# Kernel optimization log

Measured on AMD Instinct MI355X. Metric: run time of the kernel, lower is better.

Reference implementation:

```python
import jax, jax.numpy as jnp
import numpy as np
from jax import lax

PATCH_SIZE = 7


def _census_weight(patch_size, dtype=jnp.float32):
    oc = patch_size * patch_size
    w = np.eye(oc).reshape((patch_size, patch_size, 1, oc))
    w = np.transpose(w, (3, 2, 0, 1))  # [oc, 1, p, p] (OIHW)
    return jnp.asarray(w, dtype=dtype)


def _transform(t, w, patch_size):
    # t: [B, C, H, W] -> grayscale [B, 1, H, W]
    g = t.mean(axis=1, keepdims=True)
    pad = patch_size // 2
    # identity conv gathers the p*p neighborhood into channels: [B, p*p, H, W]
    patches = lax.conv_general_dilated(
        g, w.astype(g.dtype), window_strides=(1, 1),
        padding=[(pad, pad), (pad, pad)],
        dimension_numbers=('NCHW', 'OIHW', 'NCHW'))
    loc_diff = patches - g
    return loc_diff / jnp.sqrt(0.81 + loc_diff ** 2)


def _valid_mask(x, patch_size):
    pad = patch_size // 2
    b, _, h, w = x.shape
    inner = jnp.ones((b, 1, h - 2 * pad, w - 2 * pad), dtype=x.dtype)
    return jnp.pad(inner, ((0, 0), (0, 0), (pad, pad), (pad, pad)))


def setup_inputs() -> dict:
    key = jax.random.key(0)
    k1, k2 = jax.random.split(key)
    x = jax.random.uniform(k1, (8, 3, 256, 256), dtype=jnp.float32)
    y = jax.random.uniform(k2, (8, 3, 256, 256), dtype=jnp.float32)
    return {"x": x, "y": y}


def reference(x, y):
    w = _census_weight(PATCH_SIZE, x.dtype)
    ld_x = _transform(x, w, PATCH_SIZE)
    ld_y = _transform(y, w, PATCH_SIZE)
    diff = ld_x - lax.stop_gradient(ld_y)  # matches .detach()
    dist = (diff ** 2 / (0.1 + diff ** 2)).mean(axis=1, keepdims=True)
    mask = _valid_mask(x, PATCH_SIZE)
    return (dist * mask).mean()
```

## Files before the change

### kernel.cpp

```cpp
#include <hip/hip_runtime.h>

#define HW    256
#define TILE  32
#define HALO  3
#define PSIDE (TILE + 2*HALO)
#define LST   40

__global__ __launch_bounds__(256, 2) void census_loss_kernel(
    const float* __restrict__ x, const float* __restrict__ y,
    float* __restrict__ out)
{
    __shared__ __attribute__((aligned(16))) float sgx[PSIDE][LST];
    __shared__ __attribute__((aligned(16))) float sgy[PSIDE][LST];

    const int b   = blockIdx.z;
    const int ti0 = blockIdx.y * TILE;
    const int tj0 = blockIdx.x * TILE;

    const float* xb = x + (size_t)b * 3 * HW * HW;
    const float* yb = y + (size_t)b * 3 * HW * HW;

    const int tid = threadIdx.x;
    const float third = 1.0f / 3.0f;

    for (int li = tid; li < PSIDE * PSIDE; li += 256) {
        int r = li / PSIDE;
        int c = li - r * PSIDE;
        int gi = ti0 + r - HALO;
        int gj = tj0 + c - HALO;
        float gx = 0.0f, gy = 0.0f;
        if ((unsigned)gi < HW && (unsigned)gj < HW) {
            int o = gi * HW + gj;
            gx = (xb[o] + xb[o + HW*HW] + xb[o + 2*HW*HW]) * third;
            gy = (yb[o] + yb[o + HW*HW] + yb[o + 2*HW*HW]) * third;
        }
        sgx[r][c] = gx;
        sgy[r][c] = gy;
    }
    __syncthreads();

    const int cq = tid & 7;
    const int R  = tid >> 3;
    const int C0 = cq * 4;

    float acc[4] = {0.0f, 0.0f, 0.0f, 0.0f};
    float cxv[4], cyv[4];

    #define ROW_BODY(AR, GETC)                                                 \
    {                                                                          \
        const float4 a0 = *(const float4*)&sgx[(AR)][C0];                      \
        const float4 a1 = *(const float4*)&sgx[(AR)][C0 + 4];                  \
        const float4 a2 = *(const float4*)&sgx[(AR)][C0 + 8];                  \
        const float4 b0 = *(const float4*)&sgy[(AR)][C0];                      \
        const float4 b1 = *(const float4*)&sgy[(AR)][C0 + 4];                  \
        const float4 b2 = *(const float4*)&sgy[(AR)][C0 + 8];                  \
        const float wx[12] = {a0.x,a0.y,a0.z,a0.w, a1.x,a1.y,a1.z,a1.w,        \
                              a2.x,a2.y,a2.z,a2.w};                            \
        const float wy[12] = {b0.x,b0.y,b0.z,b0.w, b1.x,b1.y,b1.z,b1.w,        \
                              b2.x,b2.y,b2.z,b2.w};                            \
        if (GETC) {                                                            \
            _Pragma("unroll")                                                  \
            for (int p = 0; p < 4; ++p) { cxv[p] = wx[p+3]; cyv[p] = wy[p+3]; }\
        }                                                                      \
        _Pragma("unroll")                                                      \
        for (int p = 0; p < 4; ++p) {                                          \
            _Pragma("unroll")                                                  \
            for (int dx = 0; dx < 7; ++dx) {                                   \
                float ux = wx[p + dx] - cxv[p];                                \
                float uy = wy[p + dx] - cyv[p];                                \
                float fx = ux * __builtin_amdgcn_rsqf(__builtin_fmaf(ux, ux, 0.81f)); \
                float fy = uy * __builtin_amdgcn_rsqf(__builtin_fmaf(uy, uy, 0.81f)); \
                float d  = fx - fy;                                            \
                acc[p] += __builtin_amdgcn_rcpf(__builtin_fmaf(d, d, 0.1f));   \
            }                                                                  \
        }                                                                      \
    }

    ROW_BODY(R + 3, true)
    #pragma unroll
    for (int t = 0; t < 6; ++t) {
        const int dy = (t < 3) ? t : t + 1;
        ROW_BODY(R + dy, false)
    }
    #undef ROW_BODY

    const int gi = ti0 + R;
    const bool rowok = (gi >= HALO) & (gi < HW - HALO);
    float a = 0.0f;
    #pragma unroll
    for (int p = 0; p < 4; ++p) {
        const int gj = tj0 + C0 + p;
        a += (rowok & (gj >= HALO) & (gj < HW - HALO)) ? acc[p] : 0.0f;
    }

    #pragma unroll
    for (int off = 32; off > 0; off >>= 1)
        a += __shfl_down(a, off, 64);

    __shared__ float wsum[4];
    const int lane = tid & 63;
    const int wid  = tid >> 6;
    if (lane == 0) wsum[wid] = a;
    __syncthreads();
    if (tid == 0) {
        float s = wsum[0] + wsum[1] + wsum[2] + wsum[3];
        const float scale = 1.0f / (49.0f * 8.0f * 256.0f * 256.0f);
        float contrib = -0.1f * scale * s;
        if (blockIdx.x == 0 && blockIdx.y == 0 && blockIdx.z == 0) {
            contrib += 62500.0f / 65536.0f;
        }
        atomicAdd(out, contrib);
    }
}

extern "C" void kernel_launch(void* const* d_in, const int* in_sizes, int n_in,
                              void* d_out, int out_size, void* d_ws, size_t ws_size,
                              hipStream_t stream) {
    const float* x = (const float*)d_in[0];
    const float* y = (const float*)d_in[1];
    float* out = (float*)d_out;

    hipMemsetAsync(out, 0, sizeof(float) * out_size, stream);

    dim3 grid(HW / TILE, HW / TILE, 8);
    dim3 block(256);
    census_loss_kernel<<<grid, block, 0, stream>>>(x, y, out);
}
```

Measured before the change: 78.50 us.

## Exploit pairwise symmetry of census distance to halve neighbor evaluations

The per-pair term for pixel p and offset d equals the term for pixel p+d and offset -d, so each unordered pair is computed once. The result is credited to both pixels through separate accumulators, masked by per-column and per-row validity. Only the forward half-window (3 offsets in the centre row, 3 full rows below) is evaluated, and the centre self-pair is dropped and folded into the constant term. This roughly halves the rsq/rcp transcendental work in exchange for extra accumulators, mask FMAs and register pressure.

```diff
diff --git a/kernel.cpp b/kernel.cpp
--- a/kernel.cpp
+++ b/kernel.cpp
@@ -26,11 +26,11 @@
     for (int li = tid; li < PSIDE * PSIDE; li += 256) {
         int r = li / PSIDE;
         int c = li - r * PSIDE;
-        int gi = ti0 + r - HALO;
-        int gj = tj0 + c - HALO;
+        int gi_ = ti0 + r - HALO;
+        int gj_ = tj0 + c - HALO;
         float gx = 0.0f, gy = 0.0f;
-        if ((unsigned)gi < HW && (unsigned)gj < HW) {
-            int o = gi * HW + gj;
+        if ((unsigned)gi_ < HW && (unsigned)gj_ < HW) {
+            int o = gi_ * HW + gj_;
             gx = (xb[o] + xb[o + HW*HW] + xb[o + 2*HW*HW]) * third;
             gy = (yb[o] + yb[o + HW*HW] + yb[o + 2*HW*HW]) * third;
         }
@@ -43,55 +43,91 @@
     const int R  = tid >> 3;
     const int C0 = cq * 4;
 
-    float acc[4] = {0.0f, 0.0f, 0.0f, 0.0f};
-    float cxv[4], cyv[4];
+    const int gi = ti0 + R;
 
-    #define ROW_BODY(AR, GETC)                                                 \
-    {                                                                          \
-        const float4 a0 = *(const float4*)&sgx[(AR)][C0];                      \
-        const float4 a1 = *(const float4*)&sgx[(AR)][C0 + 4];                  \
-        const float4 a2 = *(const float4*)&sgx[(AR)][C0 + 8];                  \
-        const float4 b0 = *(const float4*)&sgy[(AR)][C0];                      \
-        const float4 b1 = *(const float4*)&sgy[(AR)][C0 + 4];                  \
-        const float4 b2 = *(const float4*)&sgy[(AR)][C0 + 8];                  \
-        const float wx[12] = {a0.x,a0.y,a0.z,a0.w, a1.x,a1.y,a1.z,a1.w,        \
-                              a2.x,a2.y,a2.z,a2.w};                            \
-        const float wy[12] = {b0.x,b0.y,b0.z,b0.w, b1.x,b1.y,b1.z,b1.w,        \
-                              b2.x,b2.y,b2.z,b2.w};                            \
-        if (GETC) {                                                            \
-            _Pragma("unroll")                                                  \
-            for (int p = 0; p < 4; ++p) { cxv[p] = wx[p+3]; cyv[p] = wy[p+3]; }\
-        }                                                                      \
-        _Pragma("unroll")                                                      \
-        for (int p = 0; p < 4; ++p) {                                          \
-            _Pragma("unroll")                                                  \
-            for (int dx = 0; dx < 7; ++dx) {                                   \
-                float ux = wx[p + dx] - cxv[p];                                \
-                float uy = wy[p + dx] - cyv[p];                                \
-                float fx = ux * __builtin_amdgcn_rsqf(__builtin_fmaf(ux, ux, 0.81f)); \
-                float fy = uy * __builtin_amdgcn_rsqf(__builtin_fmaf(uy, uy, 0.81f)); \
-                float d  = fx - fy;                                            \
-                acc[p] += __builtin_amdgcn_rcpf(__builtin_fmaf(d, d, 0.1f));   \
-            }                                                                  \
-        }                                                                      \
+    float colTf[12];
+    #pragma unroll
+    for (int q = 0; q < 12; ++q) {
+        int jq = tj0 + C0 + q - 3;
+        colTf[q] = (jq >= HALO && jq < HW - HALO) ? 1.0f : 0.0f;
+    }
+    const float rowCf = (gi >= HALO && gi < HW - HALO) ? 1.0f : 0.0f;
+
+    float accC[4] = {0.f, 0.f, 0.f, 0.f};
+    float accT = 0.0f;
+    float cx[4], cy[4];
+
+    #define LOADW(AR)                                                   \
+        { const float4 a0 = *(const float4*)&sgx[(AR)][C0];             \
+          const float4 a1 = *(const float4*)&sgx[(AR)][C0 + 4];         \
+          const float4 a2 = *(const float4*)&sgx[(AR)][C0 + 8];         \
+          const float4 b0 = *(const float4*)&sgy[(AR)][C0];             \
+          const float4 b1 = *(const float4*)&sgy[(AR)][C0 + 4];         \
+          const float4 b2 = *(const float4*)&sgy[(AR)][C0 + 8];         \
+          wx[0]=a0.x; wx[1]=a0.y; wx[2]=a0.z;  wx[3]=a0.w;              \
+          wx[4]=a1.x; wx[5]=a1.y; wx[6]=a1.z;  wx[7]=a1.w;              \
+          wx[8]=a2.x; wx[9]=a2.y; wx[10]=a2.z; wx[11]=a2.w;             \
+          wy[0]=b0.x; wy[1]=b0.y; wy[2]=b0.z;  wy[3]=b0.w;              \
+          wy[4]=b1.x; wy[5]=b1.y; wy[6]=b1.z;  wy[7]=b1.w;              \
+          wy[8]=b2.x; wy[9]=b2.y; wy[10]=b2.z; wy[11]=b2.w; }
+
+    #define BODY(Q, P)                                                    \
+        { float ux = wx[Q] - cx[P];                                       \
+          float uy = wy[Q] - cy[P];                                       \
+          float fx = ux * __builtin_amdgcn_rsqf(__builtin_fmaf(ux,ux,0.81f)); \
+          float fy = uy * __builtin_amdgcn_rsqf(__builtin_fmaf(uy,uy,0.81f)); \
+          float d  = fx - fy;                                             \
+          float G  = __builtin_amdgcn_rcpf(__builtin_fmaf(d,d,0.1f));     \
+          accC[P] += G;                                                   \
+          aq[Q]   += G; }
+
+    {
+        float wx[12], wy[12];
+        LOADW(R + 3)
+        #pragma unroll
+        for (int p = 0; p < 4; ++p) { cx[p] = wx[p + 3]; cy[p] = wy[p + 3]; }
+        float aq[12];
+        #pragma unroll
+        for (int q = 0; q < 12; ++q) aq[q] = 0.0f;
+        #pragma unroll
+        for (int p = 0; p < 4; ++p) {
+            #pragma unroll
+            for (int dx = 1; dx <= 3; ++dx)
+                BODY(p + 3 + dx, p)
+        }
+        float t = 0.0f;
+        #pragma unroll
+        for (int q = 4; q <= 9; ++q) t = __builtin_fmaf(aq[q], colTf[q], t);
+        accT = __builtin_fmaf(rowCf, t, accT);
     }
 
-    ROW_BODY(R + 3, true)
     #pragma unroll
-    for (int t = 0; t < 6; ++t) {
-        const int dy = (t < 3) ? t : t + 1;
-        ROW_BODY(R + dy, false)
+    for (int ddy = 1; ddy <= 3; ++ddy) {
+        float wx[12], wy[12];
+        LOADW(R + 3 + ddy)
+        float aq[12];
+        #pragma unroll
+        for (int q = 0; q < 12; ++q) aq[q] = 0.0f;
+        #pragma unroll
+        for (int p = 0; p < 4; ++p) {
+            #pragma unroll
+            for (int dx = 0; dx <= 6; ++dx)
+                BODY(p + dx, p)
+        }
+        const int tr = gi + ddy;
+        const float rowTf = (tr >= HALO && tr < HW - HALO) ? 1.0f : 0.0f;
+        float t = 0.0f;
+        #pragma unroll
+        for (int q = 0; q <= 9; ++q) t = __builtin_fmaf(aq[q], colTf[q], t);
+        accT = __builtin_fmaf(rowTf, t, accT);
     }
-    #undef ROW_BODY
+    #undef BODY
+    #undef LOADW
 
-    const int gi = ti0 + R;
-    const bool rowok = (gi >= HALO) & (gi < HW - HALO);
-    float a = 0.0f;
+    float a = accT;
     #pragma unroll
-    for (int p = 0; p < 4; ++p) {
-        const int gj = tj0 + C0 + p;
-        a += (rowok & (gj >= HALO) & (gj < HW - HALO)) ? acc[p] : 0.0f;
-    }
+    for (int p = 0; p < 4; ++p)
+        a = __builtin_fmaf(accC[p], rowCf * colTf[p + 3], a);
 
     #pragma unroll
     for (int off = 32; off > 0; off >>= 1)
@@ -107,7 +143,7 @@
         const float scale = 1.0f / (49.0f * 8.0f * 256.0f * 256.0f);
         float contrib = -0.1f * scale * s;
         if (blockIdx.x == 0 && blockIdx.y == 0 && blockIdx.z == 0) {
-            contrib += 62500.0f / 65536.0f;
+            contrib += (48.0f * 62500.0f) / (49.0f * 65536.0f);
         }
         atomicAdd(out, contrib);
     }
```

After: 75.57 us. 1.04x faster.
